# Kernel tuning notes

Hardware: AMD Instinct MI355X
Metric: run time of the kernel (lower is better)

## Reference

```python
import jax, jax.numpy as jnp
import numpy as np

C = 1024
H = 16
EPS = 1e-5


def setup_inputs() -> dict:
    key = jax.random.key(0)
    ks = jax.random.split(key, 10)
    B, S = 2, 2048
    s = 1.0 / np.sqrt(C)
    return {
        "hidden_states": jax.random.normal(ks[0], (B, C, S), dtype=jnp.float32),
        "attention_mask": jnp.ones((B, S), dtype=jnp.int32),
        "gn_weight": jnp.ones((C,), dtype=jnp.float32),
        "gn_bias": jnp.zeros((C,), dtype=jnp.float32),
        "Wq": jax.random.normal(ks[1], (C, C), dtype=jnp.float32) * s,
        "bq": jnp.zeros((C,), dtype=jnp.float32),
        "Wk": jax.random.normal(ks[2], (C, C), dtype=jnp.float32) * s,
        "bk": jnp.zeros((C,), dtype=jnp.float32),
        "Wv": jax.random.normal(ks[3], (C, C), dtype=jnp.float32) * s,
        "bv": jnp.zeros((C,), dtype=jnp.float32),
        "Wo": jax.random.normal(ks[4], (C, C), dtype=jnp.float32) * s,
        "bo": jnp.zeros((C,), dtype=jnp.float32),
    }


def reference(hidden_states, attention_mask, gn_weight, gn_bias,
              Wq, bq, Wk, bk, Wv, bv, Wo, bo):
    # hidden_states: (B, C, S); attention_mask: (B, S)
    B, Cc, S = hidden_states.shape
    D = Cc // H
    residual = hidden_states

    # GroupNorm with 1 group: normalize over (C, S) per sample
    mean = jnp.mean(hidden_states, axis=(1, 2), keepdims=True)
    var = jnp.var(hidden_states, axis=(1, 2), keepdims=True)
    x = (hidden_states - mean) * jax.lax.rsqrt(var + EPS)
    x = x * gn_weight[None, :, None] + gn_bias[None, :, None]

    x = jnp.transpose(x, (0, 2, 1))  # (B, S, C)
    q = x @ Wq.T + bq
    k = x @ Wk.T + bk
    v = x @ Wv.T + bv

    # (B, H, S, D)
    q = q.reshape(B, S, H, D).transpose(0, 2, 1, 3)
    k = k.reshape(B, S, H, D).transpose(0, 2, 1, 3)
    v = v.reshape(B, S, H, D).transpose(0, 2, 1, 3)

    scale = 1.0 / np.sqrt(np.sqrt(D))
    scores = jnp.einsum('bhqd,bhkd->bhqk', q * scale, k * scale)
    mask = attention_mask[:, None, None, :]  # (B,1,1,S) broadcast over heads/query
    scores = jnp.where(mask == 0, -jnp.inf, scores)
    probs = jax.nn.softmax(scores, axis=-1)

    out = jnp.einsum('bhqk,bhkd->bhqd', probs, v)  # (B,H,S,D)
    out = out.transpose(0, 2, 1, 3).reshape(B, S, Cc)
    out = out @ Wo.T + bo
    out = jnp.transpose(out, (0, 2, 1))  # (B, C, S)
    return out + residual
```

## Files before the change

### kernel.cpp

```cpp
#include <hip/hip_runtime.h>
#include <hip/hip_bf16.h>

#define B_ 2
#define C_ 1024
#define S_ 2048
#define H_ 16
#define KDIM 1024

typedef __attribute__((ext_vector_type(8))) short short8_t;
typedef __attribute__((ext_vector_type(4))) float f32x4;
typedef __attribute__((ext_vector_type(16))) float f32x16;
typedef __attribute__((ext_vector_type(4))) int i32x4;

__device__ __forceinline__ void glds16(const void* g, void* l) {
  __builtin_amdgcn_global_load_lds((const __attribute__((address_space(1))) void*)g,
                                   (__attribute__((address_space(3))) void*)l, 16, 0, 0);
}

__device__ __forceinline__ unsigned short f2bf(float f) {
  __hip_bfloat16 h = __float2bfloat16(f);
  return __builtin_bit_cast(unsigned short, h);
}

__device__ __forceinline__ unsigned pkbf(float lo, float hi) {
  unsigned r;
  asm("v_cvt_pk_bf16_f32 %0, %1, %2" : "=v"(r) : "v"(lo), "v"(hi));
  return r;
}

__device__ __forceinline__ void plswap(unsigned &a, unsigned &b) {
  asm("v_permlane32_swap_b32 %0, %1" : "+v"(a), "+v"(b));
}

__device__ __forceinline__ float max3f(float a, float b, float c) {
  float r;
  asm("v_max3_f32 %0, %1, %2, %3" : "=v"(r) : "v"(a), "v"(b), "v"(c));
  return r;
}

__device__ __forceinline__ float max16v(const f32x16& v) {
  float a = max3f(v[0], v[1], v[2]);
  float b = max3f(v[3], v[4], v[5]);
  float c = max3f(v[6], v[7], v[8]);
  float d = max3f(v[9], v[10], v[11]);
  float e = max3f(v[12], v[13], v[14]);
  float f = max3f(a, b, v[15]);
  float g = max3f(c, d, e);
  return fmaxf(f, g);
}

__global__ __launch_bounds__(256) void cvt_w4(const float* __restrict__ a,
                                              const float* __restrict__ b,
                                              const float* __restrict__ c,
                                              const float* __restrict__ d,
                                              unsigned short* __restrict__ o) {
  int g = blockIdx.x >> 10;
  const float* src = (g == 0) ? a : (g == 1) ? b : (g == 2) ? c : d;
  int i = (blockIdx.x & 1023) * 256 + threadIdx.x;
  float4 v = ((const float4*)src)[i];
  short4 r;
  r.x = (short)f2bf(v.x); r.y = (short)f2bf(v.y);
  r.z = (short)f2bf(v.z); r.w = (short)f2bf(v.w);
  ((short4*)(o))[(size_t)g * 262144 + i] = r;
}

__global__ __launch_bounds__(256) void stats1(const float* __restrict__ x,
                                              float2* __restrict__ part) {
  int bid = blockIdx.x;
  int b = bid >> 8, chunk = bid & 255;
  const float4* p = (const float4*)(x + (size_t)b*(C_*S_) + (size_t)chunk*8192);
  int t = threadIdx.x;
  float s = 0.f, q = 0.f;
#pragma unroll
  for (int i = 0; i < 8; ++i) {
    float4 v = p[t + i*256];
    s += v.x + v.y + v.z + v.w;
    q += v.x*v.x + v.y*v.y + v.z*v.z + v.w*v.w;
  }
#pragma unroll
  for (int d = 1; d < 64; d <<= 1) { s += __shfl_xor(s, d); q += __shfl_xor(q, d); }
  __shared__ float2 wsum[4];
  if ((t & 63) == 0) wsum[t >> 6] = make_float2(s, q);
  __syncthreads();
  if (t == 0) {
    float S = 0.f, Q = 0.f;
    for (int i = 0; i < 4; ++i) { S += wsum[i].x; Q += wsum[i].y; }
    part[bid] = make_float2(S, Q);
  }
}

__global__ __launch_bounds__(256) void normt(const float* __restrict__ x,
                                             const float* __restrict__ gw,
                                             const float* __restrict__ gb,
                                             const float2* __restrict__ part,
                                             unsigned short* __restrict__ xt) {
  __shared__ short lds[64*72];
  __shared__ float2 wsum2[4];
  int bid = blockIdx.x;
  int b = bid >> 9, rem = bid & 511;
  int ct = rem >> 5, st = rem & 31;
  int t = threadIdx.x;

  float2 pv = part[b*256 + t];
  float s = pv.x, q = pv.y;
#pragma unroll
  for (int d = 1; d < 64; d <<= 1) { s += __shfl_xor(s, d); q += __shfl_xor(q, d); }
  if ((t & 63) == 0) wsum2[t >> 6] = make_float2(s, q);
  __syncthreads();
  float S = 0.f, Q = 0.f;
#pragma unroll
  for (int i = 0; i < 4; ++i) { S += wsum2[i].x; Q += wsum2[i].y; }
  const float invN = 1.0f / (float)(C_*S_);
  float mean = S * invN;
  float rstd = rsqrtf(Q * invN - mean*mean + 1e-5f);

  int r = t >> 2, seg = t & 3;
  int c = ct*64 + r;
  float wsc = gw[c] * rstd;
  float bof = gb[c] - mean * wsc;
  const float4* src = (const float4*)(x + (size_t)b*(C_*S_) + (size_t)c*S_ + st*64 + seg*16);
#pragma unroll
  for (int j = 0; j < 4; ++j) {
    float4 v = src[j];
    int sl = seg*16 + j*4;
    lds[(sl+0)*72 + r] = (short)f2bf(v.x*wsc + bof);
    lds[(sl+1)*72 + r] = (short)f2bf(v.y*wsc + bof);
    lds[(sl+2)*72 + r] = (short)f2bf(v.z*wsc + bof);
    lds[(sl+3)*72 + r] = (short)f2bf(v.w*wsc + bof);
  }
  __syncthreads();
  int sl = t >> 2;
  __attribute__((aligned(16))) unsigned short tmp[16];
#pragma unroll
  for (int j = 0; j < 16; ++j) tmp[j] = (unsigned short)lds[sl*72 + seg*16 + j];
  unsigned short* dst = xt + ((size_t)b*S_ + st*64 + sl) * C_ + ct*64 + seg*16;
  *(short8_t*)dst       = *(const short8_t*)tmp;
  *(short8_t*)(dst + 8) = *(const short8_t*)(tmp + 8);
}

__global__ __launch_bounds__(256)
void gemm_qkv(const unsigned short* __restrict__ A,
              const unsigned short* __restrict__ Bm,
              const float* __restrict__ bq,
              const float* __restrict__ bk,
              const float* __restrict__ bv,
              unsigned short* __restrict__ outqk,
              unsigned short* __restrict__ outv) {
  __shared__ __attribute__((aligned(16))) short smem[128*128];
  short* As = smem;
  short* Bs = smem + 8192;
  int bid = blockIdx.x;
  int sbid = (bid & 7) * 96 + (bid >> 3);
  int bm = sbid / 24, bn = sbid % 24;
  int m0 = bm << 7, n0 = bn << 7;
  int t = threadIdx.x, l = t & 63, wid = t >> 6;
  int wr = wid >> 1, wc = wid & 1;

  int rsb = wid*8 + (l >> 3);
  int slot_src = (l & 7) ^ (l >> 3);
  const unsigned short* a_src = A + (size_t)(m0 + rsb) * KDIM + slot_src * 8;
  const unsigned short* b_src = Bm + (size_t)(n0 + rsb) * KDIM + slot_src * 8;
  char* adst = (char*)As + wid*1024;
  char* bdst = (char*)Bs + wid*1024;

  f32x4 acc[4][4] = {};

  for (int kt = 0; kt < KDIM; kt += 64) {
    __syncthreads();
#pragma unroll
    for (int i = 0; i < 4; ++i) {
      glds16(a_src + (size_t)(i*32)*KDIM + kt, adst + i*4096);
      glds16(b_src + (size_t)(i*32)*KDIM + kt, bdst + i*4096);
    }
    __syncthreads();
#pragma unroll
    for (int kk = 0; kk < 2; ++kk) {
      short8_t af[4], bf[4];
#pragma unroll
      for (int mi = 0; mi < 4; ++mi) {
        int row = wr*64 + mi*16 + (l & 15);
        int slot = (kk*4 + (l >> 4)) ^ (row & 7);
        af[mi] = *(const short8_t*)((const char*)As + row*128 + slot*16);
      }
#pragma unroll
      for (int ni = 0; ni < 4; ++ni) {
        int row = wc*64 + ni*16 + (l & 15);
        int slot = (kk*4 + (l >> 4)) ^ (row & 7);
        bf[ni] = *(const short8_t*)((const char*)Bs + row*128 + slot*16);
      }
#pragma unroll
      for (int mi = 0; mi < 4; ++mi)
#pragma unroll
        for (int ni = 0; ni < 4; ++ni)
          acc[mi][ni] = __builtin_amdgcn_mfma_f32_16x16x32_bf16(af[mi], bf[ni], acc[mi][ni], 0, 0, 0);
    }
  }

  if (bn < 16) {
    int gcol0 = n0 + wc*64;
    const float* bp = (gcol0 & 1024) ? bk : bq;
    unsigned short* ob = outqk + ((gcol0 & 1024) ? 4194304u : 0u);
    int hd0 = gcol0 & 1023;
#pragma unroll
    for (int mi = 0; mi < 4; ++mi)
#pragma unroll
      for (int ni = 0; ni < 4; ++ni)
#pragma unroll
        for (int r = 0; r < 4; ++r) {
          int gm = m0 + wr*64 + mi*16 + ((l >> 4) << 2) + r;
          int hd = hd0 + ni*16 + (l & 15);
          float v = acc[mi][ni][r] + bp[hd];
          size_t off = ((size_t)((gm >> 11)*H_ + (hd >> 6)) * S_ + (gm & 2047)) * 64 + (hd & 63);
          ob[off] = f2bf(v);
        }
  } else {
    int hdbase = n0 - 2048;
    __syncthreads();
#pragma unroll
    for (int ni = 0; ni < 4; ++ni) {
      int cl = wc*64 + ni*16 + (l & 15);
      float bvv = bv[hdbase + cl];
      int sw = (cl & 15) << 3;
#pragma unroll
      for (int mi = 0; mi < 4; ++mi)
#pragma unroll
        for (int r = 0; r < 4; ++r) {
          int rl = wr*64 + mi*16 + ((l >> 4) << 2) + r;
          smem[cl*128 + (rl ^ sw)] = (short)f2bf(acc[mi][ni][r] + bvv);
        }
    }
    __syncthreads();
    int b = m0 >> 11, s0 = m0 & 2047;
    int rn = t >> 1, seg = (t & 1) << 6;
    int sw = (rn & 15) << 3;
    unsigned short* dstp = outv + ((size_t)(b*1024 + hdbase + rn)) * 2048 + s0 + seg;
#pragma unroll
    for (int j = 0; j < 8; ++j) {
      const short* srcp = smem + rn*128 + ((seg + j*8) ^ sw);
      *(i32x4*)(dstp + j*8) = *(const i32x4*)srcp;
    }
  }
}

__global__ __launch_bounds__(256)
void gemm_o(const unsigned short* __restrict__ A,
            const unsigned short* __restrict__ Bm,
            const float* __restrict__ bias,
            const float* __restrict__ resid,
            float* __restrict__ outp) {
  __shared__ __attribute__((aligned(16))) short As[128*64];
  __shared__ __attribute__((aligned(16))) short Bs[128*64];
  int bid = blockIdx.x;
  int sbid = (bid & 7) * 32 + (bid >> 3);
  int bm = sbid & 7, bn = sbid >> 3;
  int m0 = bm << 7, n0 = bn << 7;
  int t = threadIdx.x, l = t & 63, wid = t >> 6;
  int wr = wid >> 1, wc = wid & 1;

  int rsb = wid*8 + (l >> 3);
  int slot_src = (l & 7) ^ (l >> 3);
  const unsigned short* a_src = A + (size_t)(m0 + rsb) * KDIM + slot_src * 8;
  const unsigned short* b_src = Bm + (size_t)(n0 + rsb) * KDIM + slot_src * 8;
  char* adst = (char*)As + wid*1024;
  char* bdst = (char*)Bs + wid*1024;

  f32x4 acc[4][4] = {};

  for (int kt = 0; kt < KDIM; kt += 64) {
    __syncthreads();
#pragma unroll
    for (int i = 0; i < 4; ++i) {
      glds16(a_src + (size_t)(i*32)*KDIM + kt, adst + i*4096);
      glds16(b_src + (size_t)(i*32)*KDIM + kt, bdst + i*4096);
    }
    __syncthreads();
#pragma unroll
    for (int kk = 0; kk < 2; ++kk) {
      short8_t af[4], bf[4];
#pragma unroll
      for (int mi = 0; mi < 4; ++mi) {
        int row = wr*64 + mi*16 + (l & 15);
        int slot = (kk*4 + (l >> 4)) ^ (row & 7);
        af[mi] = *(const short8_t*)((const char*)As + row*128 + slot*16);
      }
#pragma unroll
      for (int ni = 0; ni < 4; ++ni) {
        int row = wc*64 + ni*16 + (l & 15);
        int slot = (kk*4 + (l >> 4)) ^ (row & 7);
        bf[ni] = *(const short8_t*)((const char*)Bs + row*128 + slot*16);
      }
#pragma unroll
      for (int mi = 0; mi < 4; ++mi)
#pragma unroll
        for (int ni = 0; ni < 4; ++ni)
          acc[mi][ni] = __builtin_amdgcn_mfma_f32_16x16x32_bf16(af[mi], bf[ni], acc[mi][ni], 0, 0, 0);
    }
  }

#pragma unroll
  for (int mi = 0; mi < 4; ++mi)
#pragma unroll
    for (int ni = 0; ni < 4; ++ni)
#pragma unroll
      for (int r = 0; r < 4; ++r) {
        int gm = m0 + wr*64 + mi*16 + ((l >> 4) << 2) + r;
        int gn = n0 + wc*64 + ni*16 + (l & 15);
        float v = acc[mi][ni][r] + bias[gm];
        size_t off = (size_t)(gn >> 11) * ((size_t)C_*S_) + (size_t)gm * S_ + (gn & 2047);
        outp[off] = v + resid[off];
      }
}

__global__ __launch_bounds__(512, 4)
void attn_kernel(const unsigned short* __restrict__ Q,
                 const unsigned short* __restrict__ Kt,
                 const unsigned short* __restrict__ Vt,
                 const int* __restrict__ mask,
                 unsigned short* __restrict__ outp) {
  __shared__ __attribute__((aligned(16))) char lds[65536];
  __shared__ __attribute__((aligned(8)))  unsigned char maskb[256];
  __shared__ int tflag[32];

  int bid = blockIdx.x;
  int bid2 = (bid & 7) * 64 + (bid >> 3);
  int bh = bid2 >> 4, qt = bid2 & 15;
  int b = bh >> 4, h = bh & 15;
  int t = threadIdx.x, l = t & 63, wid = t >> 6;
  int quad = wid >> 2, qw = wid & 3;
  int hh = l >> 5;

  if (t < 256) {
    const i32x4* mp = (const i32x4*)(mask + b * S_) + t * 2;
    i32x4 m0 = mp[0], m1 = mp[1];
    unsigned by = (unsigned)(m0[0]!=0) | ((unsigned)(m0[1]!=0)<<1) | ((unsigned)(m0[2]!=0)<<2) | ((unsigned)(m0[3]!=0)<<3)
                | ((unsigned)(m1[0]!=0)<<4) | ((unsigned)(m1[1]!=0)<<5) | ((unsigned)(m1[2]!=0)<<6) | ((unsigned)(m1[3]!=0)<<7);
    maskb[t] = (unsigned char)by;
  }
  __syncthreads();
  if (t < 32) {
    unsigned long long v = ((const unsigned long long*)maskb)[t];
    tflag[t] = (v == 0xFFFFFFFFFFFFFFFFull) ? 1 : 0;
  }

  int q0 = qt*128 + qw*32;
  const unsigned short* qp = Q + ((size_t)bh * S_ + q0 + (l & 31)) * 64 + hh * 8;
  short8_t qf[4];
#pragma unroll
  for (int c = 0; c < 4; ++c) qf[c] = *(const short8_t*)(qp + c*16);

  int kbase = quad << 10;
  int row_st = qw*16 + (l >> 3);
  int slot_st = (l & 7) ^ (l >> 3);
  const unsigned short* kp = Kt + ((size_t)bh * S_ + kbase + row_st) * 64 + slot_st * 8;
  const unsigned short* vp = Vt + ((size_t)bh * 64 + row_st) * S_ + kbase + slot_st * 8;
  char* kdst = lds + quad*16384 + qw*2048 + l*16;
  char* vdst = kdst + 32768;

  unsigned ko[8];
#pragma unroll
  for (int c = 0; c < 4; ++c) {
    unsigned slot = (unsigned)((c*2 + hh) ^ (l & 7)) * 16u;
    ko[c]   = (unsigned)(quad*16384) + (unsigned)(l & 31)*128u + slot;
    ko[c+4] = ko[c] + 4096u;
  }

  const short8_t vones = {0x3F80, 0x3F80, 0x3F80, 0x3F80, 0x3F80, 0x3F80, 0x3F80, 0x3F80};
  const float SC = 0.18033688011112042f;
  float m_run = 0.f, msc = 0.f;
  f32x16 oc0 = {}, oc1 = {}, lsum = {};

  i32x4 kr0, kr1, vr0, vr1;
  kr0 = *(const i32x4*)(kp);
  kr1 = *(const i32x4*)(kp + 512);
  vr0 = *(const i32x4*)(vp);
  vr1 = *(const i32x4*)(vp + (size_t)8*S_);
  *(i32x4*)(kdst)        = kr0;
  *(i32x4*)(kdst + 1024) = kr1;
  *(i32x4*)(vdst)        = vr0;
  *(i32x4*)(vdst + 1024) = vr1;
  kr0 = *(const i32x4*)(kp + 4096);
  kr1 = *(const i32x4*)(kp + 4096 + 512);
  vr0 = *(const i32x4*)(vp + 64);
  vr1 = *(const i32x4*)(vp + 64 + (size_t)8*S_);
  const unsigned short* kn = kp + 8192;
  const unsigned short* vn = vp + 128;
  asm volatile("s_waitcnt lgkmcnt(0)" ::: "memory");
  __builtin_amdgcn_sched_barrier(0);
  __builtin_amdgcn_s_barrier();
  __builtin_amdgcn_sched_barrier(0);
  int lt = 0;

#define ATILE(BUF)                                                              \
  do {                                                                          \
    f32x16 st0 = {}, st1 = {};                                                  \
    __builtin_amdgcn_s_setprio(1);                                              \
    _Pragma("unroll")                                                           \
    for (int c = 0; c < 4; ++c) {                                               \
      short8_t kf0 = *(const short8_t*)(lds + ko[c]   + (BUF)*8192);            \
      short8_t kf1 = *(const short8_t*)(lds + ko[c+4] + (BUF)*8192);            \
      st0 = __builtin_amdgcn_mfma_f32_32x32x16_bf16(kf0, qf[c], st0, 0, 0, 0);  \
      st1 = __builtin_amdgcn_mfma_f32_32x32x16_bf16(kf1, qf[c], st1, 0, 0, 0);  \
    }                                                                           \
    __builtin_amdgcn_s_setprio(0);                                              \
    _Pragma("unroll")                                                           \
    for (int r = 0; r < 16; ++r) {                                              \
      st0[r] = __builtin_amdgcn_exp2f(fmaf(st0[r], SC, -msc));                  \
      st1[r] = __builtin_amdgcn_exp2f(fmaf(st1[r], SC, -msc));                  \
    }                                                                           \
    if (!tflag[(kbase >> 6) + lt]) {                                            \
      _Pragma("unroll")                                                         \
      for (int r = 0; r < 16; ++r) {                                            \
        int kl = kbase + lt*64 + (r & 3) + 8*(r >> 2) + 4*hh;                   \
        if (!((maskb[kl >> 3] >> (kl & 7)) & 1)) st0[r] = 0.f;                  \
        kl += 32;                                                               \
        if (!((maskb[kl >> 3] >> (kl & 7)) & 1)) st1[r] = 0.f;                  \
      }                                                                         \
    }                                                                           \
    float pmax = fmaxf(max16v(st0), max16v(st1));                               \
    short8_t pa[4];                                                             \
    {                                                                           \
      unsigned a0 = pkbf(st0[0],  st0[1]),  b0 = pkbf(st0[4],  st0[5]);         \
      unsigned a1 = pkbf(st0[2],  st0[3]),  b1 = pkbf(st0[6],  st0[7]);         \
      plswap(a0, b0); plswap(a1, b1);                                           \
      i32x4 w0 = {(int)a0, (int)a1, (int)b0, (int)b1};                          \
      pa[0] = __builtin_bit_cast(short8_t, w0);                                 \
      unsigned a2 = pkbf(st0[8],  st0[9]),  b2 = pkbf(st0[12], st0[13]);        \
      unsigned a3 = pkbf(st0[10], st0[11]), b3 = pkbf(st0[14], st0[15]);        \
      plswap(a2, b2); plswap(a3, b3);                                           \
      i32x4 w1 = {(int)a2, (int)a3, (int)b2, (int)b3};                          \
      pa[1] = __builtin_bit_cast(short8_t, w1);                                 \
      unsigned a4 = pkbf(st1[0],  st1[1]),  b4 = pkbf(st1[4],  st1[5]);         \
      unsigned a5 = pkbf(st1[2],  st1[3]),  b5 = pkbf(st1[6],  st1[7]);         \
      plswap(a4, b4); plswap(a5, b5);                                           \
      i32x4 w2 = {(int)a4, (int)a5, (int)b4, (int)b5};                          \
      pa[2] = __builtin_bit_cast(short8_t, w2);                                 \
      unsigned a6 = pkbf(st1[8],  st1[9]),  b6 = pkbf(st1[12], st1[13]);        \
      unsigned a7 = pkbf(st1[10], st1[11]), b7 = pkbf(st1[14], st1[15]);        \
      plswap(a6, b6); plswap(a7, b7);                                           \
      i32x4 w3 = {(int)a6, (int)a7, (int)b6, (int)b7};                          \
      pa[3] = __builtin_bit_cast(short8_t, w3);                                 \
    }                                                                           \
    __builtin_amdgcn_s_setprio(1);                                              \
    _Pragma("unroll")                                                           \
    for (int kc = 0; kc < 4; ++kc) {                                            \
      short8_t vf0 = *(const short8_t*)(lds + ko[kc]   + 32768 + (BUF)*8192);   \
      short8_t vf1 = *(const short8_t*)(lds + ko[kc+4] + 32768 + (BUF)*8192);   \
      oc0 = __builtin_amdgcn_mfma_f32_32x32x16_bf16(vf0, pa[kc], oc0, 0, 0, 0); \
      oc1 = __builtin_amdgcn_mfma_f32_32x32x16_bf16(vf1, pa[kc], oc1, 0, 0, 0); \
      lsum = __builtin_amdgcn_mfma_f32_32x32x16_bf16(vones, pa[kc], lsum, 0, 0, 0); \
    }                                                                           \
    __builtin_amdgcn_s_setprio(0);                                              \
    if (__any(pmax > 148.0f)) {                                                 \
      float pm = fmaxf(pmax, __shfl_xor(pmax, 32));                             \
      float smax = (__log2f(pm) + msc) / SC;                                    \
      float nm = fmaxf(m_run, smax);                                            \
      float fac = __builtin_amdgcn_exp2f((m_run - nm) * SC);                    \
      _Pragma("unroll")                                                         \
      for (int r = 0; r < 16; ++r) { oc0[r] *= fac; oc1[r] *= fac; lsum[r] *= fac; } \
      m_run = nm; msc = nm * SC;                                                \
    }                                                                           \
    if (lt < 15) {                                                              \
                                     \
      *(i32x4*)(kdst + ((BUF)^1)*8192)        = kr0;                            \
      *(i32x4*)(kdst + ((BUF)^1)*8192 + 1024) = kr1;                            \
      *(i32x4*)(vdst + ((BUF)^1)*8192)        = vr0;                            \
      *(i32x4*)(vdst + ((BUF)^1)*8192 + 1024) = vr1;                            \
      if (lt < 14) {                                                            \
        kr0 = *(const i32x4*)(kn);                                              \
        kr1 = *(const i32x4*)(kn + 512);                                        \
        vr0 = *(const i32x4*)(vn);                                              \
        vr1 = *(const i32x4*)(vn + (size_t)8*S_);                               \
        kn += 4096; vn += 64;                                                   \
      }                                                                         \
      asm volatile("s_waitcnt lgkmcnt(0)" ::: "memory");                        \
      __builtin_amdgcn_sched_barrier(0);                                        \
      __builtin_amdgcn_s_barrier();                                             \
      __builtin_amdgcn_sched_barrier(0);                                        \
    }                                                                           \
    ++lt;                                                                       \
  } while (0)

  for (int tp = 0; tp < 8; ++tp) {
    ATILE(0);
    ATILE(1);
  }
#undef ATILE

  __syncthreads();
  if (quad == 1) {
    char* obuf = lds + qw*8192 + l*128;
#pragma unroll
    for (int j = 0; j < 4; ++j) {
      f32x4 u0 = { oc0[4*j], oc0[4*j+1], oc0[4*j+2], oc0[4*j+3] };
      *(f32x4*)(obuf + ((j ^ (l & 7)) * 16)) = u0;
      f32x4 u1 = { oc1[4*j], oc1[4*j+1], oc1[4*j+2], oc1[4*j+3] };
      *(f32x4*)(obuf + (((j+4) ^ (l & 7)) * 16)) = u1;
    }
    *(float2*)(lds + 32768 + (qw*64 + l)*8) = make_float2(lsum[0], m_run);
  }
  __syncthreads();
  if (quad == 0) {
    float2 lm1 = *(const float2*)(lds + 32768 + (qw*64 + l)*8);
    float M  = fmaxf(m_run, lm1.y);
    float a0 = __builtin_amdgcn_exp2f((m_run - M) * SC);
    float a1 = __builtin_amdgcn_exp2f((lm1.y - M) * SC);
    float lc = lsum[0] * a0 + lm1.x * a1;
    float inv = 1.f / lc;
    float s0 = a0 * inv, s1 = a1 * inv;
    const char* obuf = lds + qw*8192 + l*128;
#pragma unroll
    for (int j = 0; j < 4; ++j) {
      f32x4 u0 = *(const f32x4*)(obuf + ((j ^ (l & 7)) * 16));
      oc0[4*j]   = oc0[4*j]  *s0 + u0[0]*s1;
      oc0[4*j+1] = oc0[4*j+1]*s0 + u0[1]*s1;
      oc0[4*j+2] = oc0[4*j+2]*s0 + u0[2]*s1;
      oc0[4*j+3] = oc0[4*j+3]*s0 + u0[3]*s1;
      f32x4 u1 = *(const f32x4*)(obuf + (((j+4) ^ (l & 7)) * 16));
      oc1[4*j]   = oc1[4*j]  *s0 + u1[0]*s1;
      oc1[4*j+1] = oc1[4*j+1]*s0 + u1[1]*s1;
      oc1[4*j+2] = oc1[4*j+2]*s0 + u1[2]*s1;
      oc1[4*j+3] = oc1[4*j+3]*s0 + u1[3]*s1;
    }

    unsigned short* obase = outp + ((size_t)b * S_ + q0 + (l & 31)) * C_ + h*64 + hh*8;
#pragma unroll
    for (int dt = 0; dt < 2; ++dt) {
      const f32x16& oc = dt ? oc1 : oc0;
      unsigned a0w = pkbf(oc[0],  oc[1]),  b0w = pkbf(oc[4],  oc[5]);
      unsigned a1w = pkbf(oc[2],  oc[3]),  b1w = pkbf(oc[6],  oc[7]);
      plswap(a0w, b0w); plswap(a1w, b1w);
      i32x4 w0 = {(int)a0w, (int)a1w, (int)b0w, (int)b1w};
      *(i32x4*)(obase + dt*32) = w0;
      unsigned a2w = pkbf(oc[8],  oc[9]),  b2w = pkbf(oc[12], oc[13]);
      unsigned a3w = pkbf(oc[10], oc[11]), b3w = pkbf(oc[14], oc[15]);
      plswap(a2w, b2w); plswap(a3w, b3w);
      i32x4 w1 = {(int)a2w, (int)a3w, (int)b2w, (int)b3w};
      *(i32x4*)(obase + dt*32 + 16) = w1;
    }
  }
}

extern "C" void kernel_launch(void* const* d_in, const int* in_sizes, int n_in,
                              void* d_out, int out_size, void* d_ws, size_t ws_size,
                              hipStream_t stream) {
  const float* hs = (const float*)d_in[0];
  const int*   msk = (const int*)d_in[1];
  const float* gw = (const float*)d_in[2];
  const float* gb = (const float*)d_in[3];
  const float* Wq = (const float*)d_in[4];
  const float* bq = (const float*)d_in[5];
  const float* Wk = (const float*)d_in[6];
  const float* bk = (const float*)d_in[7];
  const float* Wv = (const float*)d_in[8];
  const float* bv = (const float*)d_in[9];
  const float* Wo = (const float*)d_in[10];
  const float* bo = (const float*)d_in[11];

  char* ws = (char*)d_ws;
  float2* part  = (float2*)(ws + 256);
  unsigned short* wq_b = (unsigned short*)(ws + 8192);
  unsigned short* wk_b = wq_b + 1048576;
  unsigned short* wv_b = wk_b + 1048576;
  unsigned short* wo_b = wv_b + 1048576;
  unsigned short* x_b  = wo_b + 1048576;
  unsigned short* q_b  = x_b  + 4194304;
  unsigned short* k_b  = q_b  + 4194304;
  unsigned short* vt_b = k_b  + 4194304;
  unsigned short* ao_b = vt_b + 4194304;

  cvt_w4<<<4096, 256, 0, stream>>>(Wq, Wk, Wv, Wo, wq_b);

  stats1<<<512, 256, 0, stream>>>(hs, part);
  normt<<<1024, 256, 0, stream>>>(hs, gw, gb, part, x_b);

  gemm_qkv<<<768, 256, 0, stream>>>(x_b, wq_b, bq, bk, bv, q_b, vt_b);

  attn_kernel<<<512, 512, 0, stream>>>(q_b, k_b, vt_b, msk, ao_b);

  gemm_o<<<256, 256, 0, stream>>>(wo_b, ao_b, bo, hs, (float*)d_out);
}
```

Before: 142.1 us.

## Load attention K/V tiles directly into LDS and widen output GEMM blocks

The attention kernel stops staging K and V through registers. It issues global_load_lds copies straight into the alternate LDS buffer at the start of each tile, after a block barrier. This removes the register round-trip and the explicit LDS stores, and leaves the hardware waits to __syncthreads. Separately, gemm_o now runs with 512 threads in a 2x4 wave layout, halving each wave's N tile to raise occupancy and latency hiding. The catch is more barriers per tile, and the last attention tile prefetches data past the key range it actually uses.

```diff
diff --git a/kernel.cpp b/kernel.cpp
--- a/kernel.cpp
+++ b/kernel.cpp
@@ -242,7 +242,7 @@
   }
 }
 
-__global__ __launch_bounds__(256)
+__global__ __launch_bounds__(512)
 void gemm_o(const unsigned short* __restrict__ A,
             const unsigned short* __restrict__ Bm,
             const float* __restrict__ bias,
@@ -255,7 +255,7 @@
   int bm = sbid & 7, bn = sbid >> 3;
   int m0 = bm << 7, n0 = bn << 7;
   int t = threadIdx.x, l = t & 63, wid = t >> 6;
-  int wr = wid >> 1, wc = wid & 1;
+  int wr = wid >> 2, wc = wid & 3;
 
   int rsb = wid*8 + (l >> 3);
   int slot_src = (l & 7) ^ (l >> 3);
@@ -264,19 +264,18 @@
   char* adst = (char*)As + wid*1024;
   char* bdst = (char*)Bs + wid*1024;
 
-  f32x4 acc[4][4] = {};
+  f32x4 acc[4][2] = {};
 
   for (int kt = 0; kt < KDIM; kt += 64) {
     __syncthreads();
-#pragma unroll
-    for (int i = 0; i < 4; ++i) {
-      glds16(a_src + (size_t)(i*32)*KDIM + kt, adst + i*4096);
-      glds16(b_src + (size_t)(i*32)*KDIM + kt, bdst + i*4096);
-    }
+    glds16(a_src + kt, adst);
+    glds16(a_src + (size_t)64*KDIM + kt, adst + 8192);
+    glds16(b_src + kt, bdst);
+    glds16(b_src + (size_t)64*KDIM + kt, bdst + 8192);
     __syncthreads();
 #pragma unroll
     for (int kk = 0; kk < 2; ++kk) {
-      short8_t af[4], bf[4];
+      short8_t af[4], bf[2];
 #pragma unroll
       for (int mi = 0; mi < 4; ++mi) {
         int row = wr*64 + mi*16 + (l & 15);
@@ -284,15 +283,15 @@
         af[mi] = *(const short8_t*)((const char*)As + row*128 + slot*16);
       }
 #pragma unroll
-      for (int ni = 0; ni < 4; ++ni) {
-        int row = wc*64 + ni*16 + (l & 15);
+      for (int ni = 0; ni < 2; ++ni) {
+        int row = wc*32 + ni*16 + (l & 15);
         int slot = (kk*4 + (l >> 4)) ^ (row & 7);
         bf[ni] = *(const short8_t*)((const char*)Bs + row*128 + slot*16);
       }
 #pragma unroll
       for (int mi = 0; mi < 4; ++mi)
 #pragma unroll
-        for (int ni = 0; ni < 4; ++ni)
+        for (int ni = 0; ni < 2; ++ni)
           acc[mi][ni] = __builtin_amdgcn_mfma_f32_16x16x32_bf16(af[mi], bf[ni], acc[mi][ni], 0, 0, 0);
     }
   }
@@ -300,11 +299,11 @@
 #pragma unroll
   for (int mi = 0; mi < 4; ++mi)
 #pragma unroll
-    for (int ni = 0; ni < 4; ++ni)
+    for (int ni = 0; ni < 2; ++ni)
 #pragma unroll
       for (int r = 0; r < 4; ++r) {
         int gm = m0 + wr*64 + mi*16 + ((l >> 4) << 2) + r;
-        int gn = n0 + wc*64 + ni*16 + (l & 15);
+        int gn = n0 + wc*32 + ni*16 + (l & 15);
         float v = acc[mi][ni][r] + bias[gm];
         size_t off = (size_t)(gn >> 11) * ((size_t)C_*S_) + (size_t)gm * S_ + (gn & 2047);
         outp[off] = v + resid[off];
@@ -353,7 +352,7 @@
   int slot_st = (l & 7) ^ (l >> 3);
   const unsigned short* kp = Kt + ((size_t)bh * S_ + kbase + row_st) * 64 + slot_st * 8;
   const unsigned short* vp = Vt + ((size_t)bh * 64 + row_st) * S_ + kbase + slot_st * 8;
-  char* kdst = lds + quad*16384 + qw*2048 + l*16;
+  char* kdst = lds + quad*16384 + qw*2048;
   char* vdst = kdst + 32768;
 
   unsigned ko[8];
@@ -369,29 +368,22 @@
   float m_run = 0.f, msc = 0.f;
   f32x16 oc0 = {}, oc1 = {}, lsum = {};
 
-  i32x4 kr0, kr1, vr0, vr1;
-  kr0 = *(const i32x4*)(kp);
-  kr1 = *(const i32x4*)(kp + 512);
-  vr0 = *(const i32x4*)(vp);
-  vr1 = *(const i32x4*)(vp + (size_t)8*S_);
-  *(i32x4*)(kdst)        = kr0;
-  *(i32x4*)(kdst + 1024) = kr1;
-  *(i32x4*)(vdst)        = vr0;
-  *(i32x4*)(vdst + 1024) = vr1;
-  kr0 = *(const i32x4*)(kp + 4096);
-  kr1 = *(const i32x4*)(kp + 4096 + 512);
-  vr0 = *(const i32x4*)(vp + 64);
-  vr1 = *(const i32x4*)(vp + 64 + (size_t)8*S_);
-  const unsigned short* kn = kp + 8192;
-  const unsigned short* vn = vp + 128;
-  asm volatile("s_waitcnt lgkmcnt(0)" ::: "memory");
-  __builtin_amdgcn_sched_barrier(0);
-  __builtin_amdgcn_s_barrier();
-  __builtin_amdgcn_sched_barrier(0);
+  glds16(kp,                kdst);
+  glds16(kp + 8*64,         kdst + 1024);
+  glds16(vp,                vdst);
+  glds16(vp + (size_t)8*S_, vdst + 1024);
+  const unsigned short* kn = kp + 64*64;
+  const unsigned short* vn = vp + 64;
   int lt = 0;
 
 #define ATILE(BUF)                                                              \
   do {                                                                          \
+    __syncthreads();                                                            \
+    glds16(kn,                kdst + ((BUF)^1)*8192);                           \
+    glds16(kn + 8*64,         kdst + ((BUF)^1)*8192 + 1024);                    \
+    glds16(vn,                vdst + ((BUF)^1)*8192);                           \
+    glds16(vn + (size_t)8*S_, vdst + ((BUF)^1)*8192 + 1024);                    \
+    kn += 4096; vn += 64;                                                       \
     f32x16 st0 = {}, st1 = {};                                                  \
     __builtin_amdgcn_s_setprio(1);                                              \
     _Pragma("unroll")                                                           \
@@ -459,24 +451,6 @@
       for (int r = 0; r < 16; ++r) { oc0[r] *= fac; oc1[r] *= fac; lsum[r] *= fac; } \
       m_run = nm; msc = nm * SC;                                                \
     }                                                                           \
-    if (lt < 15) {                                                              \
-                                     \
-      *(i32x4*)(kdst + ((BUF)^1)*8192)        = kr0;                            \
-      *(i32x4*)(kdst + ((BUF)^1)*8192 + 1024) = kr1;                            \
-      *(i32x4*)(vdst + ((BUF)^1)*8192)        = vr0;                            \
-      *(i32x4*)(vdst + ((BUF)^1)*8192 + 1024) = vr1;                            \
-      if (lt < 14) {                                                            \
-        kr0 = *(const i32x4*)(kn);                                              \
-        kr1 = *(const i32x4*)(kn + 512);                                        \
-        vr0 = *(const i32x4*)(vn);                                              \
-        vr1 = *(const i32x4*)(vn + (size_t)8*S_);                               \
-        kn += 4096; vn += 64;                                                   \
-      }                                                                         \
-      asm volatile("s_waitcnt lgkmcnt(0)" ::: "memory");                        \
-      __builtin_amdgcn_sched_barrier(0);                                        \
-      __builtin_amdgcn_s_barrier();                                             \
-      __builtin_amdgcn_sched_barrier(0);                                        \
-    }                                                                           \
     ++lt;                                                                       \
   } while (0)
 
@@ -577,5 +551,5 @@
 
   attn_kernel<<<512, 512, 0, stream>>>(q_b, k_b, vt_b, msk, ao_b);
 
-  gemm_o<<<256, 256, 0, stream>>>(wo_b, ao_b, bo, hs, (float*)d_out);
-}
+  gemm_o<<<256, 512, 0, stream>>>(wo_b, ao_b, bo, hs, (float*)d_out);
+}
```

Result: faster. 128.5 us (-9.6%).
